# Kernel optimization log

Measured on AMD Instinct MI355X. Metric: run time of the kernel, lower is better.

## Reference

```python
import jax, jax.numpy as jnp
import numpy as np

EPS = 1e-5  # InstanceNorm2d default eps (affine=False, biased var)

def setup_inputs() -> dict:
    key = jax.random.key(0)
    ks = jax.random.split(key, 16)
    B, N, KV, H = 16, 196, 960, 4
    chs = [64, 128, 256, 512]
    inp = {}
    inp['emb0'] = jax.random.normal(ks[0], (B, N, chs[0]), jnp.float32)
    inp['emb1'] = jax.random.normal(ks[1], (B, N, chs[1]), jnp.float32)
    inp['emb2'] = jax.random.normal(ks[2], (B, N, chs[2]), jnp.float32)
    inp['emb3'] = jax.random.normal(ks[3], (B, N, chs[3]), jnp.float32)
    inp['emb_all'] = jax.random.normal(ks[4], (B, N, KV), jnp.float32)
    for i, ch in enumerate(chs):
        inp[f'Wq{i}'] = jax.random.normal(ks[5 + i], (H, ch, ch), jnp.float32) * (1.0 / np.sqrt(ch))
        inp[f'Wo{i}'] = jax.random.normal(ks[9 + i], (ch, ch), jnp.float32) * (1.0 / np.sqrt(ch))
    inp['Wk'] = jax.random.normal(ks[13], (H, KV, KV), jnp.float32) * (1.0 / np.sqrt(KV))
    inp['Wv'] = jax.random.normal(ks[14], (H, KV, KV), jnp.float32) * (1.0 / np.sqrt(KV))
    return inp

def _attend(emb, Wq, Wo, K, V, inv_sqrt_kv):
    # Q: per-head Linear(ch,ch) then transpose(-1,-2) -> [B,H,ch,N]
    Q = jnp.einsum('bnc,hdc->bhdn', emb, Wq)
    # scores: [B,H,ch,KV]
    scores = jnp.einsum('bhdn,bhnj->bhdj', Q, K) * inv_sqrt_kv
    # InstanceNorm2d over the (ch, KV) plane per (batch, head), no affine
    m = scores.mean(axis=(-2, -1), keepdims=True)
    v = scores.var(axis=(-2, -1), keepdims=True)
    probs = jax.nn.softmax((scores - m) * jax.lax.rsqrt(v + EPS), axis=-1)
    # ctx = (probs @ V^T).permute(0,3,2,1).mean(dim=3) -> mean over heads: [B,N,ch]
    ctx = jnp.einsum('bhdj,bhnj->bnd', probs, V) / probs.shape[1]
    # out projection: nn.Linear(ch,ch) -> x @ Wo^T
    return jnp.einsum('bnd,ed->bne', ctx, Wo)

def reference(emb0, emb1, emb2, emb3, emb_all, Wq0, Wq1, Wq2, Wq3, Wk, Wv, Wo0, Wo1, Wo2, Wo3):
    KV = emb_all.shape[-1]
    inv_sqrt_kv = jnp.float32(1.0 / np.sqrt(KV))
    # multi-head K/V: stacked per-head Linear(KV,KV) -> [B,H,N,KV]
    K = jnp.einsum('bnk,hjk->bhnj', emb_all, Wk)
    V = jnp.einsum('bnk,hjk->bhnj', emb_all, Wv)
    o0 = _attend(emb0, Wq0, Wo0, K, V, inv_sqrt_kv)
    o1 = _attend(emb1, Wq1, Wo1, K, V, inv_sqrt_kv)
    o2 = _attend(emb2, Wq2, Wo2, K, V, inv_sqrt_kv)
    o3 = _attend(emb3, Wq3, Wo3, K, V, inv_sqrt_kv)
    return (o0, o1, o2, o3)
```

## Files before the change

### kernel.cpp

```cpp
#include <hip/hip_runtime.h>

typedef _Float16 half_t;
typedef _Float16 h8 __attribute__((ext_vector_type(8)));
typedef _Float16 h4 __attribute__((ext_vector_type(4)));
typedef float f4v __attribute__((ext_vector_type(4)));

__device__ __forceinline__ int div196(int m) { return (m * 21400) >> 22; }

struct PrepArgs {
    const float* src[15];
    half_t* dst[15];
    int n[15];
    int mode[15];
    int lg2[15];
};

__global__ __launch_bounds__(256) void prep_k(PrepArgs a)
{
    const int seg = blockIdx.y;
    const int i8 = (blockIdx.x * 256 + threadIdx.x) * 8;
    if (i8 >= a.n[seg]) return;
    const float* s = a.src[seg] + i8;
    f4v v0 = *(const f4v*)s;
    f4v v1 = *(const f4v*)(s + 4);
    h8 o;
    o[0] = (half_t)v0[0]; o[1] = (half_t)v0[1]; o[2] = (half_t)v0[2]; o[3] = (half_t)v0[3];
    o[4] = (half_t)v1[0]; o[5] = (half_t)v1[1]; o[6] = (half_t)v1[2]; o[7] = (half_t)v1[3];
    if (a.mode[seg] == 0) {
        *(h8*)(a.dst[seg] + i8) = o;
    } else {
        const int lg = a.lg2[seg], ch = 1 << lg;
        const int e = i8 >> lg, d = i8 & (ch - 1);
        half_t* base = a.dst[seg] + ((long long)e << (lg + 2)) + d;
        #pragma unroll
        for (int r = 0; r < 4; ++r) *(h8*)(base + r * ch) = o;
    }
}

__device__ __forceinline__ h8 ldtile(const half_t* __restrict__ base, int row, int kb,
                                     int ld, int rowLim, int Klim)
{
    h8 v = {0, 0, 0, 0, 0, 0, 0, 0};
    if (row >= rowLim) return v;
    const half_t* p = base + (long long)row * ld + kb;
    if (kb + 8 <= Klim) return *(const h8*)p;
    #pragma unroll
    for (int e = 0; e < 8; ++e) if (kb + e < Klim) v[e] = p[e];
    return v;
}

struct BP {
    const half_t* A[4]; const half_t* B[4]; void* C[4];
    int Mlim[4], Nlim[4], Klim[4], nKt[4], lda[4], ldb[4], ldc[4];
    int divA[4]; long long sAhi[4], sAlo[4];
    int divB[4]; long long sBhi[4], sBlo[4];
    int divC[4]; long long sChi[4], sClo[4];
    long long tStrB[4]; int tComp[4];
    float alpha[4];
    int mT[4], nT[4];
    int cumEnd[3];
    int totW;
};

template<int OUT>
__global__ __launch_bounds__(128)
void gemm_b(BP P)
{
    __shared__ __align__(16) half_t SM[64 * 72];
    half_t (*As)[32] = (half_t(*)[32])SM;
    half_t (*Bs)[32] = (half_t(*)[32])(SM + 2048);

    int b = blockIdx.x;
    int s = 0, basev = 0;
    #pragma unroll
    for (int i = 0; i < 3; ++i) if (b >= P.cumEnd[i]) { s = i + 1; basev = P.cumEnd[i]; }
    b -= basev;
    const int mTl = P.mT[s], nTl = P.nT[s];
    const int mt = b % mTl;
    const int t2 = b / mTl;
    const int nt = t2 % nTl;
    const int z  = t2 / nTl;

    const half_t* A  = P.A[s] + (long long)(z / P.divA[s]) * P.sAhi[s] + (long long)(z % P.divA[s]) * P.sAlo[s];
    const half_t* Bp = P.B[s] + (long long)(z / P.divB[s]) * P.sBhi[s] + (long long)(z % P.divB[s]) * P.sBlo[s];
    const int Mlim = P.Mlim[s], Klim = P.Klim[s], nKt = P.nKt[s];
    const int lda = P.lda[s], ldb = P.ldb[s], ldc = P.ldc[s];
    const float alpha = P.alpha[s];
    const int m0 = mt * 64, n0 = nt * 64;
    const int tid = threadIdx.x;
    const int lane = tid & 63, w = tid >> 6;
    const int l15 = lane & 15, q = lane >> 4;

    const int r0 = tid >> 2, kg = tid & 3;
    const int r1 = r0 + 32;

    f4v acc[4][2];
    #pragma unroll
    for (int i = 0; i < 4; ++i)
        #pragma unroll
        for (int j = 0; j < 2; ++j) acc[i][j] = (f4v){0.f, 0.f, 0.f, 0.f};

    for (int kt = 0; kt < nKt; ++kt) {
        const int kb = kt * 32 + kg * 8;
        h8 a0 = ldtile(A, m0 + r0, kb, lda, Mlim, Klim);
        h8 a1 = ldtile(A, m0 + r1, kb, lda, Mlim, Klim);
        h8 b0 = ldtile(Bp, n0 + r0, kb, ldb, 1 << 30, Klim);
        h8 b1 = ldtile(Bp, n0 + r1, kb, ldb, 1 << 30, Klim);
        __syncthreads();
        *(h8*)&As[r0][kg * 8] = a0;
        *(h8*)&As[r1][kg * 8] = a1;
        *(h8*)&Bs[r0][kg * 8] = b0;
        *(h8*)&Bs[r1][kg * 8] = b1;
        __syncthreads();
        h8 af[4], bf[2];
        #pragma unroll
        for (int mti = 0; mti < 4; ++mti) af[mti] = *(h8*)&As[mti * 16 + l15][q * 8];
        #pragma unroll
        for (int nti = 0; nti < 2; ++nti) bf[nti] = *(h8*)&Bs[w * 32 + nti * 16 + l15][q * 8];
        #pragma unroll
        for (int mti = 0; mti < 4; ++mti)
            #pragma unroll
            for (int nti = 0; nti < 2; ++nti)
                acc[mti][nti] = __builtin_amdgcn_mfma_f32_16x16x32_f16(af[mti], bf[nti], acc[mti][nti], 0, 0, 0);
    }

    if (OUT == 0) {
        float* Cz = (float*)P.C[s] + (long long)(z / P.divC[s]) * P.sChi[s] + (long long)(z % P.divC[s]) * P.sClo[s];
        #pragma unroll
        for (int mti = 0; mti < 4; ++mti)
            #pragma unroll
            for (int r = 0; r < 4; ++r) {
                const int row = m0 + mti * 16 + q * 4 + r;
                if (row < Mlim) {
                    #pragma unroll
                    for (int nti = 0; nti < 2; ++nti) {
                        const int col = n0 + w * 32 + nti * 16 + l15;
                        Cz[(long long)row * ldc + col] = acc[mti][nti][r] * alpha;
                    }
                }
            }
    } else {
        __syncthreads();
        half_t (*Tt)[72] = (half_t(*)[72])SM;
        #pragma unroll
        for (int mti = 0; mti < 4; ++mti)
            #pragma unroll
            for (int nti = 0; nti < 2; ++nti) {
                h4 pk;
                #pragma unroll
                for (int r = 0; r < 4; ++r) pk[r] = (half_t)(acc[mti][nti][r] * alpha);
                *(h4*)&Tt[w * 32 + nti * 16 + l15][mti * 16 + q * 4] = pk;
            }
        __syncthreads();
        half_t* Cz = (half_t*)P.C[s] + (long long)(z / P.divC[s]) * P.sChi[s] + (long long)(z % P.divC[s]) * P.sClo[s];
        const long long tStrB = P.tStrB[s];
        const int jl = tid >> 1, mh = (tid & 1) * 32;
        #pragma unroll
        for (int g = 0; g < 4; ++g) {
            const int ml = mh + g * 8;
            const int mg = m0 + ml;
            h8 v = *(h8*)&Tt[jl][ml];
            if (P.tComp[s]) {
                const int b0 = div196(mg), b1 = div196(mg + 7);
                if (b0 == b1 && mg + 8 <= Mlim) {
                    half_t* rp = Cz + (long long)b0 * tStrB + (long long)(n0 + jl) * ldc + (mg - 196 * b0);
                    h4 lo = {v[0], v[1], v[2], v[3]};
                    h4 hi = {v[4], v[5], v[6], v[7]};
                    *(h4*)rp = lo;
                    *(h4*)(rp + 4) = hi;
                } else {
                    #pragma unroll
                    for (int e = 0; e < 8; ++e) {
                        const int m = mg + e;
                        if (m < Mlim) {
                            const int bb = div196(m);
                            Cz[(long long)bb * tStrB + (long long)(n0 + jl) * ldc + (m - 196 * bb)] = v[e];
                        }
                    }
                }
            } else {
                if (mg + 8 <= Mlim) {
                    *(h8*)(Cz + (long long)(n0 + jl) * ldc + mg) = v;
                } else {
                    #pragma unroll
                    for (int e = 0; e < 8; ++e)
                        if (mg + e < Mlim) Cz[(long long)(n0 + jl) * ldc + mg + e] = v[e];
                }
            }
        }
    }
}

template<int OUT>
__global__ __launch_bounds__(256)
void gemm_w(BP P)
{
    __shared__ __align__(16) half_t SMEM[128 * 80];
    half_t (*As)[40] = (half_t(*)[40])SMEM;
    half_t (*Bs)[40] = (half_t(*)[40])(SMEM + 128 * 40);

    const int per = gridDim.x >> 3;
    int wk = (blockIdx.x & 7) * per + (blockIdx.x >> 3);
    if (wk >= P.totW) return;
    int s = 0, basev = 0;
    #pragma unroll
    for (int i = 0; i < 3; ++i) if (wk >= P.cumEnd[i]) { s = i + 1; basev = P.cumEnd[i]; }
    wk -= basev;
    const int mTl = P.mT[s], nTl = P.nT[s];
    const int mt = wk % mTl;
    const int t2 = wk / mTl;
    const int nt = t2 % nTl;
    const int z  = t2 / nTl;

    const half_t* A  = P.A[s] + (long long)(z / P.divA[s]) * P.sAhi[s] + (long long)(z % P.divA[s]) * P.sAlo[s];
    const half_t* Bp = P.B[s] + (long long)(z / P.divB[s]) * P.sBhi[s] + (long long)(z % P.divB[s]) * P.sBlo[s];
    const int Mlim = P.Mlim[s], Nlim = P.Nlim[s], Klim = P.Klim[s], nKt = P.nKt[s];
    const int lda = P.lda[s], ldb = P.ldb[s], ldc = P.ldc[s];
    const float alpha = P.alpha[s];
    const int m0 = mt * 128, n0 = nt * 128;
    const int tid = threadIdx.x;
    const int lane = tid & 63, wv = tid >> 6;
    const int wm = wv & 1, wn = wv >> 1;
    const int l15 = lane & 15, q = lane >> 4;

    const int r0 = tid >> 2, kg = tid & 3;

    f4v acc[4][4];
    #pragma unroll
    for (int i = 0; i < 4; ++i)
        #pragma unroll
        for (int j = 0; j < 4; ++j) acc[i][j] = (f4v){0.f, 0.f, 0.f, 0.f};

    for (int kt = 0; kt < nKt; ++kt) {
        const int kb = kt * 32 + kg * 8;
        h8 a0 = ldtile(A, m0 + r0, kb, lda, Mlim, Klim);
        h8 a1 = ldtile(A, m0 + r0 + 64, kb, lda, Mlim, Klim);
        h8 b0 = ldtile(Bp, n0 + r0, kb, ldb, Nlim, Klim);
        h8 b1 = ldtile(Bp, n0 + r0 + 64, kb, ldb, Nlim, Klim);
        __syncthreads();
        *(h8*)&As[r0][kg * 8] = a0;
        *(h8*)&As[r0 + 64][kg * 8] = a1;
        *(h8*)&Bs[r0][kg * 8] = b0;
        *(h8*)&Bs[r0 + 64][kg * 8] = b1;
        __syncthreads();
        h8 af[4], bf[4];
        #pragma unroll
        for (int mi = 0; mi < 4; ++mi) af[mi] = *(h8*)&As[wm * 64 + mi * 16 + l15][q * 8];
        #pragma unroll
        for (int ni = 0; ni < 4; ++ni) bf[ni] = *(h8*)&Bs[wn * 64 + ni * 16 + l15][q * 8];
        #pragma unroll
        for (int mi = 0; mi < 4; ++mi)
            #pragma unroll
            for (int ni = 0; ni < 4; ++ni)
                acc[mi][ni] = __builtin_amdgcn_mfma_f32_16x16x32_f16(af[mi], bf[ni], acc[mi][ni], 0, 0, 0);
    }

    if (OUT == 1) {
        half_t* Cz = (half_t*)P.C[s] + (long long)(z / P.divC[s]) * P.sChi[s] + (long long)(z % P.divC[s]) * P.sClo[s];
        #pragma unroll
        for (int mi = 0; mi < 4; ++mi)
            #pragma unroll
            for (int r = 0; r < 4; ++r) {
                const int row = m0 + wm * 64 + mi * 16 + q * 4 + r;
                if (row < Mlim) {
                    #pragma unroll
                    for (int ni = 0; ni < 4; ++ni) {
                        const int col = n0 + wn * 64 + ni * 16 + l15;
                        if (col < Nlim) Cz[(long long)row * ldc + col] = (half_t)(acc[mi][ni][r] * alpha);
                    }
                }
            }
    } else {
        half_t (*Tt)[72] = (half_t(*)[72])SMEM;
        half_t* Cz = (half_t*)P.C[s] + (long long)(z / P.divC[s]) * P.sChi[s] + (long long)(z % P.divC[s]) * P.sClo[s];
        const long long tStrB = P.tStrB[s];
        const int jl = tid >> 1, mh = (tid & 1) * 32;
        #pragma unroll
        for (int p = 0; p < 2; ++p) {
            __syncthreads();
            if (wm == p) {
                #pragma unroll
                for (int mi = 0; mi < 4; ++mi)
                    #pragma unroll
                    for (int ni = 0; ni < 4; ++ni) {
                        h4 pk;
                        #pragma unroll
                        for (int r = 0; r < 4; ++r) pk[r] = (half_t)(acc[mi][ni][r] * alpha);
                        *(h4*)&Tt[wn * 64 + ni * 16 + l15][mi * 16 + q * 4] = pk;
                    }
            }
            __syncthreads();
            const int n = n0 + jl;
            if (n < Nlim) {
                #pragma unroll
                for (int g = 0; g < 4; ++g) {
                    const int ml = mh + g * 8;
                    const int mg = m0 + p * 64 + ml;
                    h8 v = *(h8*)&Tt[jl][ml];
                    const int b0 = div196(mg), b1 = div196(mg + 7);
                    if (b0 == b1 && mg + 8 <= Mlim) {
                        half_t* rp = Cz + (long long)b0 * tStrB + (long long)n * ldc + (mg - 196 * b0);
                        h4 lo = {v[0], v[1], v[2], v[3]};
                        h4 hi = {v[4], v[5], v[6], v[7]};
                        *(h4*)rp = lo;
                        *(h4*)(rp + 4) = hi;
                    } else {
                        #pragma unroll
                        for (int e = 0; e < 8; ++e) {
                            const int m = mg + e;
                            if (m < Mlim) {
                                const int bb = div196(m);
                                Cz[(long long)bb * tStrB + (long long)n * ldc + (m - 196 * bb)] = v[e];
                            }
                        }
                    }
                }
            }
        }
    }
}

struct ScP {
    const half_t* Qt[4];
    const half_t* KT;
    half_t* C[4];
    float* Part[4];
    int Mlim[4];
    long long sA[4], sC[4];
    float alpha;
};

__global__ __launch_bounds__(256)
void gemm_s(ScP P)
{
    __shared__ __align__(16) half_t As[128][232];
    __shared__ __align__(16) half_t Bs[128][72];
    __shared__ float red[8];

    const int per = gridDim.x >> 3;
    int wk = (blockIdx.x & 7) * per + (blockIdx.x >> 3);
    const int z = wk >> 3, r = wk & 7;
    int s, mt;
    if (r < 1)      { s = 0; mt = 0; }
    else if (r < 2) { s = 1; mt = 0; }
    else if (r < 4) { s = 2; mt = r - 2; }
    else            { s = 3; mt = r - 4; }
    const int b = z >> 2, h = z & 3;

    const half_t* A = P.Qt[s] + (long long)z * P.sA[s] + (long long)mt * 128 * 208;
    const half_t* B = P.KT + (long long)h * 3194880 + (long long)b * 199680;
    const int rowLim = P.Mlim[s] - mt * 128;
    const float alpha = P.alpha;

    const int tid = threadIdx.x;
    const int lane = tid & 63, wv = tid >> 6;
    const int wm = wv & 1, wn = wv >> 1;
    const int l15 = lane & 15, q = lane >> 4;
    const int r0 = tid >> 2, kg = tid & 3;

    #pragma unroll
    for (int c = 0; c < 7; ++c) {
        const int kb = c * 32 + kg * 8;
        h8 a0 = ldtile(A, r0, kb, 208, rowLim, 196);
        h8 a1 = ldtile(A, r0 + 64, kb, 208, rowLim, 196);
        *(h8*)&As[r0][kb] = a0;
        *(h8*)&As[r0 + 64][kb] = a1;
    }

    half_t* Cz = P.C[s] + (long long)z * P.sC[s] + (long long)mt * 128 * 960;
    float sv = 0.f, qq = 0.f;

    for (int nt = 0; nt < 8; ++nt) {
        f4v acc[4][4];
        #pragma unroll
        for (int i = 0; i < 4; ++i)
            #pragma unroll
            for (int j = 0; j < 4; ++j) acc[i][j] = (f4v){0.f, 0.f, 0.f, 0.f};

        const int j0 = nt * 128;
        #pragma unroll
        for (int c2 = 0; c2 < 4; ++c2) {
            h8 b00 = ldtile(B, j0 + r0,      c2 * 64 + kg * 8,      208, 960, 196);
            h8 b01 = ldtile(B, j0 + r0,      c2 * 64 + 32 + kg * 8, 208, 960, 196);
            h8 b10 = ldtile(B, j0 + r0 + 64, c2 * 64 + kg * 8,      208, 960, 196);
            h8 b11 = ldtile(B, j0 + r0 + 64, c2 * 64 + 32 + kg * 8, 208, 960, 196);
            __syncthreads();
            *(h8*)&Bs[r0][kg * 8] = b00;
            *(h8*)&Bs[r0][32 + kg * 8] = b01;
            *(h8*)&Bs[r0 + 64][kg * 8] = b10;
            *(h8*)&Bs[r0 + 64][32 + kg * 8] = b11;
            __syncthreads();
            const int nkk = (c2 < 3) ? 2 : 1;
            for (int kk = 0; kk < nkk; ++kk) {
                const int base = c2 * 64 + kk * 32;
                h8 af[4], bf[4];
                #pragma unroll
                for (int mi = 0; mi < 4; ++mi) af[mi] = *(h8*)&As[wm * 64 + mi * 16 + l15][base + q * 8];
                #pragma unroll
                for (int ni = 0; ni < 4; ++ni) bf[ni] = *(h8*)&Bs[wn * 64 + ni * 16 + l15][kk * 32 + q * 8];
                #pragma unroll
                for (int mi = 0; mi < 4; ++mi)
                    #pragma unroll
                    for (int ni = 0; ni < 4; ++ni)
                        acc[mi][ni] = __builtin_amdgcn_mfma_f32_16x16x32_f16(af[mi], bf[ni], acc[mi][ni], 0, 0, 0);
            }
        }
        #pragma unroll
        for (int mi = 0; mi < 4; ++mi)
            #pragma unroll
            for (int rr = 0; rr < 4; ++rr) {
                const int rowl = wm * 64 + mi * 16 + q * 4 + rr;
                #pragma unroll
                for (int ni = 0; ni < 4; ++ni) {
                    const int col = j0 + wn * 64 + ni * 16 + l15;
                    const float v = acc[mi][ni][rr] * alpha;
                    sv += v; qq += v * v;
                    if (rowl < rowLim && col < 960)
                        Cz[(long long)rowl * 960 + col] = (half_t)v;
                }
            }
    }

    #pragma unroll
    for (int o = 32; o > 0; o >>= 1) {
        sv += __shfl_down(sv, o, 64);
        qq += __shfl_down(qq, o, 64);
    }
    if (lane == 0) { red[wv] = sv; red[4 + wv] = qq; }
    __syncthreads();
    if (tid == 0) {
        float* PO = P.Part[s] + (long long)z * 240 + mt * 2;
        PO[0] = red[0] + red[1] + red[2] + red[3];
        PO[1] = red[4] + red[5] + red[6] + red[7];
    }
}

struct CtxP {
    const half_t* V;
    const half_t* S[4];
    half_t* C[4];
    const float* Part[4];
    int ch[4];
    int nPart[4];
    float pinv[4];
};

__global__ __launch_bounds__(256)
void ctx_k(CtxP P)
{
    __shared__ __align__(16) half_t As[128][40];
    __shared__ __align__(16) half_t Bs[128][40];
    __shared__ float denomP[128][4];
    __shared__ float denom[128];

    const int per = gridDim.x >> 3;
    int wk = (blockIdx.x & 7) * per + (blockIdx.x >> 3);
    const int z = wk >> 4;
    const int r = wk & 15;
    int s, mt, nt;
    if (r < 2)      { s = 0; mt = r;            nt = 0; }
    else if (r < 4) { s = 1; mt = r - 2;        nt = 0; }
    else if (r < 8) { s = 2; mt = (r - 4) >> 1; nt = (r - 4) & 1; }
    else            { s = 3; mt = (r - 8) >> 2; nt = (r - 8) & 3; }
    const int b = z >> 2, h = z & 3;
    const int chS = P.ch[s];

    const float* part = P.Part[s] + (long long)z * 240;
    float Ssum = 0.f, Qsum = 0.f;
    for (int i = 0; i < P.nPart[s]; ++i) { Ssum += part[i * 2]; Qsum += part[i * 2 + 1]; }
    const float mn = Ssum * P.pinv[s];
    const float rs = rsqrtf(fmaxf(Qsum * P.pinv[s] - mn * mn, 0.f) + 1e-5f);

    const half_t* Av  = P.V + (long long)h * 3010560 + (long long)b * 188160;
    const half_t* Bsc = P.S[s] + (long long)z * 960 * chS;
    const int m0 = mt * 128, n0 = nt * 128;

    const int tid = threadIdx.x;
    const int lane = tid & 63, wv = tid >> 6;
    const int wm = wv & 1, wn = wv >> 1;
    const int l15 = lane & 15, q = lane >> 4;
    const int r0 = tid >> 2, kg = tid & 3;
    const int d0 = n0 + r0, d1 = n0 + r0 + 64;

    f4v acc[4][4];
    #pragma unroll
    for (int i = 0; i < 4; ++i)
        #pragma unroll
        for (int j = 0; j < 4; ++j) acc[i][j] = (f4v){0.f, 0.f, 0.f, 0.f};

    float ds0 = 0.f, ds1 = 0.f;

    for (int kt = 0; kt < 30; ++kt) {
        const int kb = kt * 32 + kg * 8;
        h8 a0 = ldtile(Av, m0 + r0, kb, 960, 196, 960);
        h8 a1 = ldtile(Av, m0 + r0 + 64, kb, 960, 196, 960);
        h8 s0 = {0,0,0,0,0,0,0,0}, s1 = {0,0,0,0,0,0,0,0};
        if (d0 < chS) s0 = *(const h8*)(Bsc + (long long)d0 * 960 + kb);
        if (d1 < chS) s1 = *(const h8*)(Bsc + (long long)d1 * 960 + kb);
        __syncthreads();
        h8 e0 = {0,0,0,0,0,0,0,0}, e1 = {0,0,0,0,0,0,0,0};
        if (d0 < chS) {
            #pragma unroll
            for (int e = 0; e < 8; ++e) { float ev = __expf((float)s0[e] * rs); ds0 += ev; e0[e] = (half_t)ev; }
        }
        if (d1 < chS) {
            #pragma unroll
            for (int e = 0; e < 8; ++e) { float ev = __expf((float)s1[e] * rs); ds1 += ev; e1[e] = (half_t)ev; }
        }
        *(h8*)&As[r0][kg * 8] = a0;
        *(h8*)&As[r0 + 64][kg * 8] = a1;
        *(h8*)&Bs[r0][kg * 8] = e0;
        *(h8*)&Bs[r0 + 64][kg * 8] = e1;
        __syncthreads();
        h8 af[4], bf[4];
        #pragma unroll
        for (int mi = 0; mi < 4; ++mi) af[mi] = *(h8*)&As[wm * 64 + mi * 16 + l15][q * 8];
        #pragma unroll
        for (int ni = 0; ni < 4; ++ni) bf[ni] = *(h8*)&Bs[wn * 64 + ni * 16 + l15][q * 8];
        #pragma unroll
        for (int mi = 0; mi < 4; ++mi)
            #pragma unroll
            for (int ni = 0; ni < 4; ++ni)
                acc[mi][ni] = __builtin_amdgcn_mfma_f32_16x16x32_f16(af[mi], bf[ni], acc[mi][ni], 0, 0, 0);
    }

    denomP[r0][kg] = ds0;
    denomP[r0 + 64][kg] = ds1;
    __syncthreads();
    if (tid < 128) denom[tid] = denomP[tid][0] + denomP[tid][1] + denomP[tid][2] + denomP[tid][3];
    __syncthreads();

    half_t* Cz = P.C[s] + (long long)b * 784 * chS + (long long)h * chS;
    const int ldc = 4 * chS;
    #pragma unroll
    for (int ni = 0; ni < 4; ++ni) {
        const int coll = wn * 64 + ni * 16 + l15;
        const int col = n0 + coll;
        if (col < chS) {
            const float sc = 0.25f / denom[coll];
            #pragma unroll
            for (int mi = 0; mi < 4; ++mi)
                #pragma unroll
                for (int rr = 0; rr < 4; ++rr) {
                    const int row = m0 + wm * 64 + mi * 16 + q * 4 + rr;
                    if (row < 196)
                        Cz[(long long)row * ldc + col] = (half_t)(acc[mi][ni][rr] * sc);
                }
        }
    }
}

extern "C" void kernel_launch(void* const* d_in, const int* in_sizes, int n_in,
                              void* d_out, int out_size, void* d_ws, size_t ws_size,
                              hipStream_t stream)
{
    const float* emb[4]  = {(const float*)d_in[0], (const float*)d_in[1],
                            (const float*)d_in[2], (const float*)d_in[3]};
    const float* emb_all = (const float*)d_in[4];
    const float* Wq[4]   = {(const float*)d_in[5], (const float*)d_in[7],
                            (const float*)d_in[9], (const float*)d_in[11]};
    const float* Wo[4]   = {(const float*)d_in[6], (const float*)d_in[8],
                            (const float*)d_in[10], (const float*)d_in[12]};
    const float* Wk = (const float*)d_in[13];
    const float* Wv = (const float*)d_in[14];
    float* out = (float*)d_out;

    half_t* hb = (half_t*)d_ws;
    half_t* EAh = hb;
    half_t* Eh  = EAh + 3010560;
    half_t* Wkh = Eh  + 3010560;
    half_t* Wvh = Wkh + 3686400;
    half_t* Wqh = Wvh + 3686400;
    half_t* Wo4 = Wqh + 1392640;
    half_t* KT  = Wo4 + 1392640;
    half_t* Vh  = KT  + 12779520;
    half_t* QtT = Vh  + 12042240;
    half_t* Ctx = QtT + 12779520;
    half_t* Sch = Ctx + 12042240;
    float*  Part = (float*)(Sch + 58982400);

    const int  chs[4]   = {64, 128, 256, 512};
    const int  lg2c[4]  = {6, 7, 8, 9};
    const long long offE[4]   = {0, 200704, 602112, 1404928};
    const long long offQ[4]   = {0, 16384, 81920, 344064};
    const long long offQt[4]  = {0, 851968, 2555904, 5963776};
    const long long offSc[4]  = {0, 3932160, 11796480, 27525120};
    const long long offCtx[4] = {0, 802816, 2408448, 5619712};
    const long long ooff[4]   = {0, 200704, 602112, 1404928};
    const float inv_sqrt_kv = 0.03227486121839514f;

    PrepArgs pa;
    pa.src[0] = emb_all; pa.dst[0] = EAh; pa.n[0] = 3010560; pa.mode[0] = 0; pa.lg2[0] = 0;
    for (int i = 0; i < 4; ++i) {
        pa.src[1 + i] = emb[i]; pa.dst[1 + i] = Eh + offE[i];
        pa.n[1 + i] = (int)(3136LL * chs[i]); pa.mode[1 + i] = 0; pa.lg2[1 + i] = 0;
    }
    pa.src[5] = Wk; pa.dst[5] = Wkh; pa.n[5] = 3686400; pa.mode[5] = 0; pa.lg2[5] = 0;
    pa.src[6] = Wv; pa.dst[6] = Wvh; pa.n[6] = 3686400; pa.mode[6] = 0; pa.lg2[6] = 0;
    for (int i = 0; i < 4; ++i) {
        pa.src[7 + i] = Wq[i]; pa.dst[7 + i] = Wqh + offQ[i];
        pa.n[7 + i] = 4 * chs[i] * chs[i]; pa.mode[7 + i] = 0; pa.lg2[7 + i] = 0;
        pa.src[11 + i] = Wo[i]; pa.dst[11 + i] = Wo4 + offQ[i];
        pa.n[11 + i] = chs[i] * chs[i]; pa.mode[11 + i] = 1; pa.lg2[11 + i] = lg2c[i];
    }
    prep_k<<<dim3(1800, 15), 256, 0, stream>>>(pa);

    {
        BP p{};
        p.A[0] = EAh; p.B[0] = Wkh; p.C[0] = KT;
        p.Mlim[0] = 3136; p.Nlim[0] = 960; p.Klim[0] = 960; p.nKt[0] = 30;
        p.lda[0] = 960; p.ldb[0] = 960; p.ldc[0] = 208;
        p.divA[0] = 1; p.sAhi[0] = 0; p.sAlo[0] = 0;
        p.divB[0] = 1; p.sBhi[0] = 921600; p.sBlo[0] = 0;
        p.divC[0] = 1; p.sChi[0] = 3194880; p.sClo[0] = 0;
        p.tStrB[0] = 199680; p.tComp[0] = 1; p.alpha[0] = 1.0f;
        p.mT[0] = 25; p.nT[0] = 8;
        p.cumEnd[0] = p.cumEnd[1] = p.cumEnd[2] = 800;
        p.totW = 800;
        gemm_w<2><<<800, 256, 0, stream>>>(p);
    }
    {
        BP p{};
        p.A[0] = EAh; p.B[0] = Wvh; p.C[0] = Vh;
        p.Mlim[0] = 3136; p.Nlim[0] = 960; p.Klim[0] = 960; p.nKt[0] = 30;
        p.lda[0] = 960; p.ldb[0] = 960; p.ldc[0] = 960;
        p.divA[0] = 1; p.sAhi[0] = 0; p.sAlo[0] = 0;
        p.divB[0] = 1; p.sBhi[0] = 921600; p.sBlo[0] = 0;
        p.divC[0] = 1; p.sChi[0] = 3010560; p.sClo[0] = 0;
        p.alpha[0] = 1.0f;
        p.mT[0] = 25; p.nT[0] = 8;
        p.cumEnd[0] = p.cumEnd[1] = p.cumEnd[2] = 800;
        p.totW = 800;
        gemm_w<1><<<800, 256, 0, stream>>>(p);
    }

    {
        BP p{};
        int cum = 0;
        for (int s = 0; s < 4; ++s) {
            const int ch = chs[s];
            p.A[s] = Eh + offE[s]; p.B[s] = Wqh + offQ[s]; p.C[s] = QtT + offQt[s];
            p.Mlim[s] = 196; p.Nlim[s] = ch; p.Klim[s] = ch; p.nKt[s] = ch / 32;
            p.lda[s] = ch; p.ldb[s] = ch; p.ldc[s] = 208;
            p.divA[s] = 4; p.sAhi[s] = 196LL * ch; p.sAlo[s] = 0;
            p.divB[s] = 4; p.sBhi[s] = 0; p.sBlo[s] = (long long)ch * ch;
            p.divC[s] = 1; p.sChi[s] = 208LL * ch; p.sClo[s] = 0;
            p.tStrB[s] = 0; p.tComp[s] = 0; p.alpha[s] = 1.0f;
            p.mT[s] = 4; p.nT[s] = ch / 64;
            cum += 4 * (ch / 64) * 64;
            if (s < 3) p.cumEnd[s] = cum;
        }
        p.totW = 3840;
        gemm_b<2><<<3840, 128, 0, stream>>>(p);
    }

    {
        ScP p{};
        for (int s = 0; s < 4; ++s) {
            p.Qt[s] = QtT + offQt[s];
            p.C[s] = Sch + offSc[s];
            p.Part[s] = Part + (long long)s * 64 * 240;
            p.Mlim[s] = chs[s];
            p.sA[s] = 208LL * chs[s];
            p.sC[s] = 960LL * chs[s];
        }
        p.KT = KT;
        p.alpha = inv_sqrt_kv;
        gemm_s<<<512, 256, 0, stream>>>(p);
    }

    {
        CtxP p{};
        p.V = Vh;
        const int nP[4] = {1, 1, 2, 4};
        for (int s = 0; s < 4; ++s) {
            p.S[s] = Sch + offSc[s];
            p.C[s] = Ctx + offCtx[s];
            p.Part[s] = Part + (long long)s * 64 * 240;
            p.ch[s] = chs[s];
            p.nPart[s] = nP[s];
            p.pinv[s] = 1.0f / (chs[s] * 960);
        }
        ctx_k<<<1024, 256, 0, stream>>>(p);
    }

    {
        BP p{};
        int cum = 0;
        for (int s = 0; s < 4; ++s) {
            const int ch = chs[s];
            p.A[s] = Ctx + offCtx[s]; p.B[s] = Wo4 + offQ[s]; p.C[s] = out + ooff[s];
            p.Mlim[s] = 196; p.Nlim[s] = ch; p.Klim[s] = 4 * ch; p.nKt[s] = ch / 8;
            p.lda[s] = 4 * ch; p.ldb[s] = 4 * ch; p.ldc[s] = ch;
            p.divA[s] = 1; p.sAhi[s] = 784LL * ch; p.sAlo[s] = 0;
            p.divB[s] = 1; p.sBhi[s] = 0; p.sBlo[s] = 0;
            p.divC[s] = 1; p.sChi[s] = 196LL * ch; p.sClo[s] = 0;
            p.tStrB[s] = 0; p.tComp[s] = 0; p.alpha[s] = 1.0f;
            p.mT[s] = 4; p.nT[s] = ch / 64;
            cum += 4 * (ch / 64) * 16;
            if (s < 3) p.cumEnd[s] = cum;
        }
        p.totW = 960;
        gemm_b<0><<<960, 128, 0, stream>>>(p);
    }
}
```

Before: 452.7 us.

## Merge K, V and Q projection GEMMs into one launch; prefetch tiles in ctx kernel

Merges the separate K-projection, V-projection and per-scale Q-projection GEMM launches into a single gemm_w launch with six segments. A runtime outMode and tComp flag now select each segment's store path, and the Q GEMMs switch to 128x128 tiles. Separately, the ctx kernel now register-prefetches the next K-tile of V and scores while the current tile's MMAs run. The merge removes two launches and lets the small Q GEMMs fill the GPU alongside the large ones. The cost is runtime branching in the epilogue, larger tiles that waste work on the small Q shapes, and more register pressure from the prefetch.

New measurement: 432.1 us. 1.05x faster.

```diff
diff --git a/kernel.cpp b/kernel.cpp
--- a/kernel.cpp
+++ b/kernel.cpp
@@ -50,19 +50,19 @@
 }
 
 struct BP {
-    const half_t* A[4]; const half_t* B[4]; void* C[4];
-    int Mlim[4], Nlim[4], Klim[4], nKt[4], lda[4], ldb[4], ldc[4];
-    int divA[4]; long long sAhi[4], sAlo[4];
-    int divB[4]; long long sBhi[4], sBlo[4];
-    int divC[4]; long long sChi[4], sClo[4];
-    long long tStrB[4]; int tComp[4];
-    float alpha[4];
-    int mT[4], nT[4];
-    int cumEnd[3];
+    const half_t* A[6]; const half_t* B[6]; void* C[6];
+    int Mlim[6], Nlim[6], Klim[6], nKt[6], lda[6], ldb[6], ldc[6];
+    int divA[6]; long long sAhi[6], sAlo[6];
+    int divB[6]; long long sBhi[6], sBlo[6];
+    int divC[6]; long long sChi[6], sClo[6];
+    long long tStrB[6]; int tComp[6];
+    int outMode[6];
+    float alpha[6];
+    int mT[6], nT[6];
+    int cumEnd[5];
     int totW;
 };
 
-template<int OUT>
 __global__ __launch_bounds__(128)
 void gemm_b(BP P)
 {
@@ -73,7 +73,7 @@
     int b = blockIdx.x;
     int s = 0, basev = 0;
     #pragma unroll
-    for (int i = 0; i < 3; ++i) if (b >= P.cumEnd[i]) { s = i + 1; basev = P.cumEnd[i]; }
+    for (int i = 0; i < 5; ++i) if (b >= P.cumEnd[i]) { s = i + 1; basev = P.cumEnd[i]; }
     b -= basev;
     const int mTl = P.mT[s], nTl = P.nT[s];
     const int mt = b % mTl;
@@ -124,74 +124,22 @@
                 acc[mti][nti] = __builtin_amdgcn_mfma_f32_16x16x32_f16(af[mti], bf[nti], acc[mti][nti], 0, 0, 0);
     }
 
-    if (OUT == 0) {
-        float* Cz = (float*)P.C[s] + (long long)(z / P.divC[s]) * P.sChi[s] + (long long)(z % P.divC[s]) * P.sClo[s];
-        #pragma unroll
-        for (int mti = 0; mti < 4; ++mti)
-            #pragma unroll
-            for (int r = 0; r < 4; ++r) {
-                const int row = m0 + mti * 16 + q * 4 + r;
-                if (row < Mlim) {
-                    #pragma unroll
-                    for (int nti = 0; nti < 2; ++nti) {
-                        const int col = n0 + w * 32 + nti * 16 + l15;
-                        Cz[(long long)row * ldc + col] = acc[mti][nti][r] * alpha;
-                    }
+    float* Cz = (float*)P.C[s] + (long long)(z / P.divC[s]) * P.sChi[s] + (long long)(z % P.divC[s]) * P.sClo[s];
+    #pragma unroll
+    for (int mti = 0; mti < 4; ++mti)
+        #pragma unroll
+        for (int r = 0; r < 4; ++r) {
+            const int row = m0 + mti * 16 + q * 4 + r;
+            if (row < Mlim) {
+                #pragma unroll
+                for (int nti = 0; nti < 2; ++nti) {
+                    const int col = n0 + w * 32 + nti * 16 + l15;
+                    Cz[(long long)row * ldc + col] = acc[mti][nti][r] * alpha;
                 }
             }
-    } else {
-        __syncthreads();
-        half_t (*Tt)[72] = (half_t(*)[72])SM;
-        #pragma unroll
-        for (int mti = 0; mti < 4; ++mti)
-            #pragma unroll
-            for (int nti = 0; nti < 2; ++nti) {
-                h4 pk;
-                #pragma unroll
-                for (int r = 0; r < 4; ++r) pk[r] = (half_t)(acc[mti][nti][r] * alpha);
-                *(h4*)&Tt[w * 32 + nti * 16 + l15][mti * 16 + q * 4] = pk;
-            }
-        __syncthreads();
-        half_t* Cz = (half_t*)P.C[s] + (long long)(z / P.divC[s]) * P.sChi[s] + (long long)(z % P.divC[s]) * P.sClo[s];
-        const long long tStrB = P.tStrB[s];
-        const int jl = tid >> 1, mh = (tid & 1) * 32;
-        #pragma unroll
-        for (int g = 0; g < 4; ++g) {
-            const int ml = mh + g * 8;
-            const int mg = m0 + ml;
-            h8 v = *(h8*)&Tt[jl][ml];
-            if (P.tComp[s]) {
-                const int b0 = div196(mg), b1 = div196(mg + 7);
-                if (b0 == b1 && mg + 8 <= Mlim) {
-                    half_t* rp = Cz + (long long)b0 * tStrB + (long long)(n0 + jl) * ldc + (mg - 196 * b0);
-                    h4 lo = {v[0], v[1], v[2], v[3]};
-                    h4 hi = {v[4], v[5], v[6], v[7]};
-                    *(h4*)rp = lo;
-                    *(h4*)(rp + 4) = hi;
-                } else {
-                    #pragma unroll
-                    for (int e = 0; e < 8; ++e) {
-                        const int m = mg + e;
-                        if (m < Mlim) {
-                            const int bb = div196(m);
-                            Cz[(long long)bb * tStrB + (long long)(n0 + jl) * ldc + (m - 196 * bb)] = v[e];
-                        }
-                    }
-                }
-            } else {
-                if (mg + 8 <= Mlim) {
-                    *(h8*)(Cz + (long long)(n0 + jl) * ldc + mg) = v;
-                } else {
-                    #pragma unroll
-                    for (int e = 0; e < 8; ++e)
-                        if (mg + e < Mlim) Cz[(long long)(n0 + jl) * ldc + mg + e] = v[e];
-                }
-            }
-        }
-    }
+        }
 }
 
-template<int OUT>
 __global__ __launch_bounds__(256)
 void gemm_w(BP P)
 {
@@ -204,7 +152,7 @@
     if (wk >= P.totW) return;
     int s = 0, basev = 0;
     #pragma unroll
-    for (int i = 0; i < 3; ++i) if (wk >= P.cumEnd[i]) { s = i + 1; basev = P.cumEnd[i]; }
+    for (int i = 0; i < 5; ++i) if (wk >= P.cumEnd[i]) { s = i + 1; basev = P.cumEnd[i]; }
     wk -= basev;
     const int mTl = P.mT[s], nTl = P.nT[s];
     const int mt = wk % mTl;
@@ -255,7 +203,7 @@
                 acc[mi][ni] = __builtin_amdgcn_mfma_f32_16x16x32_f16(af[mi], bf[ni], acc[mi][ni], 0, 0, 0);
     }
 
-    if (OUT == 1) {
+    if (P.outMode[s] == 1) {
         half_t* Cz = (half_t*)P.C[s] + (long long)(z / P.divC[s]) * P.sChi[s] + (long long)(z % P.divC[s]) * P.sClo[s];
         #pragma unroll
         for (int mi = 0; mi < 4; ++mi)
@@ -297,21 +245,31 @@
                     const int ml = mh + g * 8;
                     const int mg = m0 + p * 64 + ml;
                     h8 v = *(h8*)&Tt[jl][ml];
-                    const int b0 = div196(mg), b1 = div196(mg + 7);
-                    if (b0 == b1 && mg + 8 <= Mlim) {
-                        half_t* rp = Cz + (long long)b0 * tStrB + (long long)n * ldc + (mg - 196 * b0);
-                        h4 lo = {v[0], v[1], v[2], v[3]};
-                        h4 hi = {v[4], v[5], v[6], v[7]};
-                        *(h4*)rp = lo;
-                        *(h4*)(rp + 4) = hi;
+                    if (P.tComp[s]) {
+                        const int b0 = div196(mg), b1 = div196(mg + 7);
+                        if (b0 == b1 && mg + 8 <= Mlim) {
+                            half_t* rp = Cz + (long long)b0 * tStrB + (long long)n * ldc + (mg - 196 * b0);
+                            h4 lo = {v[0], v[1], v[2], v[3]};
+                            h4 hi = {v[4], v[5], v[6], v[7]};
+                            *(h4*)rp = lo;
+                            *(h4*)(rp + 4) = hi;
+                        } else {
+                            #pragma unroll
+                            for (int e = 0; e < 8; ++e) {
+                                const int m = mg + e;
+                                if (m < Mlim) {
+                                    const int bb = div196(m);
+                                    Cz[(long long)bb * tStrB + (long long)n * ldc + (m - 196 * bb)] = v[e];
+                                }
+                            }
+                        }
                     } else {
-                        #pragma unroll
-                        for (int e = 0; e < 8; ++e) {
-                            const int m = mg + e;
-                            if (m < Mlim) {
-                                const int bb = div196(m);
-                                Cz[(long long)bb * tStrB + (long long)n * ldc + (m - 196 * bb)] = v[e];
-                            }
+                        if (mg + 8 <= Mlim) {
+                            *(h8*)(Cz + (long long)n * ldc + mg) = v;
+                        } else {
+                            #pragma unroll
+                            for (int e = 0; e < 8; ++e)
+                                if (mg + e < Mlim) Cz[(long long)n * ldc + mg + e] = v[e];
                         }
                     }
                 }
@@ -481,6 +439,7 @@
     const int l15 = lane & 15, q = lane >> 4;
     const int r0 = tid >> 2, kg = tid & 3;
     const int d0 = n0 + r0, d1 = n0 + r0 + 64;
+    const bool ok0 = d0 < chS, ok1 = d1 < chS;
 
     f4v acc[4][4];
     #pragma unroll
@@ -490,28 +449,36 @@
 
     float ds0 = 0.f, ds1 = 0.f;
 
+    h8 a0n = ldtile(Av, m0 + r0, kg * 8, 960, 196, 960);
+    h8 a1n = ldtile(Av, m0 + r0 + 64, kg * 8, 960, 196, 960);
+    h8 s0n = {0,0,0,0,0,0,0,0}, s1n = {0,0,0,0,0,0,0,0};
+    if (ok0) s0n = *(const h8*)(Bsc + (long long)d0 * 960 + kg * 8);
+    if (ok1) s1n = *(const h8*)(Bsc + (long long)d1 * 960 + kg * 8);
+
     for (int kt = 0; kt < 30; ++kt) {
-        const int kb = kt * 32 + kg * 8;
-        h8 a0 = ldtile(Av, m0 + r0, kb, 960, 196, 960);
-        h8 a1 = ldtile(Av, m0 + r0 + 64, kb, 960, 196, 960);
-        h8 s0 = {0,0,0,0,0,0,0,0}, s1 = {0,0,0,0,0,0,0,0};
-        if (d0 < chS) s0 = *(const h8*)(Bsc + (long long)d0 * 960 + kb);
-        if (d1 < chS) s1 = *(const h8*)(Bsc + (long long)d1 * 960 + kb);
+        h8 e0 = {0,0,0,0,0,0,0,0}, e1 = {0,0,0,0,0,0,0,0};
+        if (ok0) {
+            #pragma unroll
+            for (int e = 0; e < 8; ++e) { float ev = __expf((float)s0n[e] * rs); ds0 += ev; e0[e] = (half_t)ev; }
+        }
+        if (ok1) {
+            #pragma unroll
+            for (int e = 0; e < 8; ++e) { float ev = __expf((float)s1n[e] * rs); ds1 += ev; e1[e] = (half_t)ev; }
+        }
+        h8 a0c = a0n, a1c = a1n;
         __syncthreads();
-        h8 e0 = {0,0,0,0,0,0,0,0}, e1 = {0,0,0,0,0,0,0,0};
-        if (d0 < chS) {
-            #pragma unroll
-            for (int e = 0; e < 8; ++e) { float ev = __expf((float)s0[e] * rs); ds0 += ev; e0[e] = (half_t)ev; }
-        }
-        if (d1 < chS) {
-            #pragma unroll
-            for (int e = 0; e < 8; ++e) { float ev = __expf((float)s1[e] * rs); ds1 += ev; e1[e] = (half_t)ev; }
-        }
-        *(h8*)&As[r0][kg * 8] = a0;
-        *(h8*)&As[r0 + 64][kg * 8] = a1;
+        *(h8*)&As[r0][kg * 8] = a0c;
+        *(h8*)&As[r0 + 64][kg * 8] = a1c;
         *(h8*)&Bs[r0][kg * 8] = e0;
         *(h8*)&Bs[r0 + 64][kg * 8] = e1;
         __syncthreads();
+        if (kt < 29) {
+            const int kb = (kt + 1) * 32 + kg * 8;
+            a0n = ldtile(Av, m0 + r0, kb, 960, 196, 960);
+            a1n = ldtile(Av, m0 + r0 + 64, kb, 960, 196, 960);
+            if (ok0) s0n = *(const h8*)(Bsc + (long long)d0 * 960 + kb);
+            if (ok1) s1n = *(const h8*)(Bsc + (long long)d1 * 960 + kb);
+        }
         h8 af[4], bf[4];
         #pragma unroll
         for (int mi = 0; mi < 4; ++mi) af[mi] = *(h8*)&As[wm * 64 + mi * 16 + l15][q * 8];
@@ -613,45 +580,32 @@
         p.divA[0] = 1; p.sAhi[0] = 0; p.sAlo[0] = 0;
         p.divB[0] = 1; p.sBhi[0] = 921600; p.sBlo[0] = 0;
         p.divC[0] = 1; p.sChi[0] = 3194880; p.sClo[0] = 0;
-        p.tStrB[0] = 199680; p.tComp[0] = 1; p.alpha[0] = 1.0f;
+        p.tStrB[0] = 199680; p.tComp[0] = 1; p.outMode[0] = 2; p.alpha[0] = 1.0f;
         p.mT[0] = 25; p.nT[0] = 8;
-        p.cumEnd[0] = p.cumEnd[1] = p.cumEnd[2] = 800;
-        p.totW = 800;
-        gemm_w<2><<<800, 256, 0, stream>>>(p);
-    }
-    {
-        BP p{};
-        p.A[0] = EAh; p.B[0] = Wvh; p.C[0] = Vh;
-        p.Mlim[0] = 3136; p.Nlim[0] = 960; p.Klim[0] = 960; p.nKt[0] = 30;
-        p.lda[0] = 960; p.ldb[0] = 960; p.ldc[0] = 960;
-        p.divA[0] = 1; p.sAhi[0] = 0; p.sAlo[0] = 0;
-        p.divB[0] = 1; p.sBhi[0] = 921600; p.sBlo[0] = 0;
-        p.divC[0] = 1; p.sChi[0] = 3010560; p.sClo[0] = 0;
-        p.alpha[0] = 1.0f;
-        p.mT[0] = 25; p.nT[0] = 8;
-        p.cumEnd[0] = p.cumEnd[1] = p.cumEnd[2] = 800;
-        p.totW = 800;
-        gemm_w<1><<<800, 256, 0, stream>>>(p);
-    }
-
-    {
-        BP p{};
+        p.A[1] = EAh; p.B[1] = Wvh; p.C[1] = Vh;
+        p.Mlim[1] = 3136; p.Nlim[1] = 960; p.Klim[1] = 960; p.nKt[1] = 30;
+        p.lda[1] = 960; p.ldb[1] = 960; p.ldc[1] = 960;
+        p.divA[1] = 1; p.sAhi[1] = 0; p.sAlo[1] = 0;
+        p.divB[1] = 1; p.sBhi[1] = 921600; p.sBlo[1] = 0;
+        p.divC[1] = 1; p.sChi[1] = 3010560; p.sClo[1] = 0;
+        p.tStrB[1] = 0; p.tComp[1] = 0; p.outMode[1] = 1; p.alpha[1] = 1.0f;
+        p.mT[1] = 25; p.nT[1] = 8;
+        for (int i = 0; i < 4; ++i) {
+            const int sl = 2 + i, ch = chs[i];
+            p.A[sl] = Eh + offE[i]; p.B[sl] = Wqh + offQ[i]; p.C[sl] = QtT + offQt[i];
+            p.Mlim[sl] = 196; p.Nlim[sl] = ch; p.Klim[sl] = ch; p.nKt[sl] = ch / 32;
+            p.lda[sl] = ch; p.ldb[sl] = ch; p.ldc[sl] = 208;
+            p.divA[sl] = 4; p.sAhi[sl] = 196LL * ch; p.sAlo[sl] = 0;
+            p.divB[sl] = 4; p.sBhi[sl] = 0; p.sBlo[sl] = (long long)ch * ch;
+            p.divC[sl] = 1; p.sChi[sl] = 208LL * ch; p.sClo[sl] = 0;
+            p.tStrB[sl] = 0; p.tComp[sl] = 0; p.outMode[sl] = 2; p.alpha[sl] = 1.0f;
+            p.mT[sl] = 2; p.nT[sl] = (ch + 127) / 128;
+        }
         int cum = 0;
-        for (int s = 0; s < 4; ++s) {
-            const int ch = chs[s];
-            p.A[s] = Eh + offE[s]; p.B[s] = Wqh + offQ[s]; p.C[s] = QtT + offQt[s];
-            p.Mlim[s] = 196; p.Nlim[s] = ch; p.Klim[s] = ch; p.nKt[s] = ch / 32;
-            p.lda[s] = ch; p.ldb[s] = ch; p.ldc[s] = 208;
-            p.divA[s] = 4; p.sAhi[s] = 196LL * ch; p.sAlo[s] = 0;
-            p.divB[s] = 4; p.sBhi[s] = 0; p.sBlo[s] = (long long)ch * ch;
-            p.divC[s] = 1; p.sChi[s] = 208LL * ch; p.sClo[s] = 0;
-            p.tStrB[s] = 0; p.tComp[s] = 0; p.alpha[s] = 1.0f;
-            p.mT[s] = 4; p.nT[s] = ch / 64;
-            cum += 4 * (ch / 64) * 64;
-            if (s < 3) p.cumEnd[s] = cum;
-        }
-        p.totW = 3840;
-        gemm_b<2><<<3840, 128, 0, stream>>>(p);
+        const int blocks[6] = {800, 800, 128, 128, 256, 512};
+        for (int sl = 0; sl < 6; ++sl) { cum += blocks[sl]; if (sl < 5) p.cumEnd[sl] = cum; }
+        p.totW = cum;
+        gemm_w<<<2624, 256, 0, stream>>>(p);
     }
 
     {
@@ -695,12 +649,13 @@
             p.divA[s] = 1; p.sAhi[s] = 784LL * ch; p.sAlo[s] = 0;
             p.divB[s] = 1; p.sBhi[s] = 0; p.sBlo[s] = 0;
             p.divC[s] = 1; p.sChi[s] = 196LL * ch; p.sClo[s] = 0;
-            p.tStrB[s] = 0; p.tComp[s] = 0; p.alpha[s] = 1.0f;
+            p.tStrB[s] = 0; p.tComp[s] = 0; p.outMode[s] = 0; p.alpha[s] = 1.0f;
             p.mT[s] = 4; p.nT[s] = ch / 64;
             cum += 4 * (ch / 64) * 16;
             if (s < 3) p.cumEnd[s] = cum;
         }
-        p.totW = 960;
-        gemm_b<0><<<960, 128, 0, stream>>>(p);
+        p.cumEnd[3] = p.cumEnd[4] = cum;
+        p.totW = cum;
+        gemm_b<<<960, 128, 0, stream>>>(p);
     }
 }
```
